# Kernel optimization log

Hardware: AMD Instinct MI355X
Metric: run time of the kernel (lower is better)

Reference implementation:

```python
import jax, jax.numpy as jnp
import numpy as np

D = 128            # EMBEDDING_DIM
B = 8192           # batch
L = 5              # MAX_PLAYLIST_LENGTH
P = 100            # cross projection dim
F = 15 * D         # concat width = 1920
TABLES = {
    'T_name': 1000001, 'T_collab': 4, 'T_track_uri_can': 2262292,
    'T_n_songs': 6, 'T_n_artists': 6, 'T_n_albums': 6,
    'T_artist_name': 287711, 'T_track_uri_pl': 2262293, 'T_track_name': 1483754,
    'T_duration': 101, 'T_album_name': 571626, 'T_artist_pop': 6,
    'T_followers': 11, 'T_track_pop': 11, 'T_genres': 734685,
}


def setup_inputs() -> dict:
    key = jax.random.key(0)
    ks = iter(jax.random.split(key, 64))
    def ridx(shape, hi):
        return jax.random.randint(next(ks), shape, 0, hi, dtype=jnp.int32)
    inp = {
        'name': ridx((B,), 1000001), 'collaborative': ridx((B,), 4),
        'track_uri_can': ridx((B,), 2262292), 'n_songs_pl': ridx((B,), 6),
        'num_artists_pl': ridx((B,), 6), 'num_albums_pl': ridx((B,), 6),
        'artist_name_pl': ridx((B, L), 287711), 'track_uri_pl': ridx((B, L), 2262293),
        'track_name_pl': ridx((B, L), 1483754), 'duration_ms_songs_pl': ridx((B, L), 101),
        'album_name_pl': ridx((B, L), 571626), 'artist_pop_pl': ridx((B, L), 6),
        'artists_followers_pl': ridx((B, L), 11), 'track_pop_pl': ridx((B, L), 11),
        'artist_genres_pl': ridx((B, L), 734685),
    }
    for nm, rows in TABLES.items():
        inp[nm] = jax.random.normal(next(ks), (rows, D), jnp.float32) * 0.05
    def glorot(k, shp):
        lim = np.sqrt(6.0 / (shp[0] + shp[1])).astype(np.float32)
        return jax.random.uniform(k, shp, jnp.float32, -lim, lim)
    inp['cross_V'] = glorot(next(ks), (F, P))
    inp['cross_U'] = glorot(next(ks), (P, F))
    inp['cross_b'] = jnp.zeros((F,), jnp.float32)
    inp['W0'] = glorot(next(ks), (F, 512)); inp['b0'] = jnp.zeros((512,), jnp.float32)
    inp['W1'] = glorot(next(ks), (512, 256)); inp['b1'] = jnp.zeros((256,), jnp.float32)
    inp['W2'] = glorot(next(ks), (256, 128)); inp['b2'] = jnp.zeros((128,), jnp.float32)
    return inp


def _masked_mean(tab, idx):
    # Embedding(mask_zero=True) + GlobalAveragePooling1D: average over idx != 0
    e = tab[idx]                                   # [B, L, D]
    m = (idx != 0).astype(e.dtype)[..., None]      # [B, L, 1]
    return (e * m).sum(1) / jnp.maximum(m.sum(1), 1.0)


def _forward(name, collaborative, track_uri_can, n_songs_pl, num_artists_pl,
             num_albums_pl, artist_name_pl, track_uri_pl, track_name_pl,
             duration_ms_songs_pl, album_name_pl, artist_pop_pl,
             artists_followers_pl, track_pop_pl, artist_genres_pl,
             T_name, T_collab, T_track_uri_can, T_n_songs, T_n_artists,
             T_n_albums, T_artist_name, T_track_uri_pl, T_track_name,
             T_duration, T_album_name, T_artist_pop, T_followers, T_track_pop,
             T_genres, cross_V, cross_U, cross_b, W0, b0, W1, b1, W2, b2):
    all_embs = jnp.concatenate([
        T_name[name], T_collab[collaborative], T_track_uri_can[track_uri_can],
        T_n_songs[n_songs_pl], T_n_artists[num_artists_pl], T_n_albums[num_albums_pl],
        _masked_mean(T_artist_name, artist_name_pl),
        _masked_mean(T_track_uri_pl, track_uri_pl),
        _masked_mean(T_track_name, track_name_pl),
        _masked_mean(T_duration, duration_ms_songs_pl),
        _masked_mean(T_album_name, album_name_pl),
        T_artist_pop[artist_pop_pl].mean(1),        # mask_zero=False -> plain mean
        T_followers[artists_followers_pl].mean(1),
        T_track_pop[track_pop_pl].mean(1),
        _masked_mean(T_genres, artist_genres_pl),
    ], axis=1)                                      # [B, 1920]
    # tfrs DCN Cross (low-rank): x0 * (U(V(x)) + b) + x, x0 == x here
    x0 = all_embs
    cross = x0 * (jnp.dot(jnp.dot(x0, cross_V), cross_U) + cross_b) + x0
    # dense tower (dropout is identity at inference)
    h = jax.nn.relu(cross @ W0 + b0)
    h = jax.nn.relu(h @ W1 + b1)
    h = h @ W2 + b2
    # tf.nn.l2_normalize(x, 1, epsilon=1e-12)
    return h * jax.lax.rsqrt(jnp.maximum(jnp.sum(h * h, 1, keepdims=True), 1e-12))


def reference(name, collaborative, track_uri_can, n_songs_pl, num_artists_pl,
              num_albums_pl, artist_name_pl, track_uri_pl, track_name_pl,
              duration_ms_songs_pl, album_name_pl, artist_pop_pl,
              artists_followers_pl, track_pop_pl, artist_genres_pl,
              T_name, T_collab, T_track_uri_can, T_n_songs, T_n_artists,
              T_n_albums, T_artist_name, T_track_uri_pl, T_track_name,
              T_duration, T_album_name, T_artist_pop, T_followers, T_track_pop,
              T_genres, cross_V, cross_U, cross_b, W0, b0, W1, b1, W2, b2):
    return _forward(name, collaborative, track_uri_can, n_songs_pl, num_artists_pl,
                    num_albums_pl, artist_name_pl, track_uri_pl, track_name_pl,
                    duration_ms_songs_pl, album_name_pl, artist_pop_pl,
                    artists_followers_pl, track_pop_pl, artist_genres_pl,
                    T_name, T_collab, T_track_uri_can, T_n_songs, T_n_artists,
                    T_n_albums, T_artist_name, T_track_uri_pl, T_track_name,
                    T_duration, T_album_name, T_artist_pop, T_followers,
                    T_track_pop, T_genres, cross_V, cross_U, cross_b,
                    W0, b0, W1, b1, W2, b2)
```

## Files before the change

kernel.cpp:

```cpp
#include <hip/hip_runtime.h>


constexpr int B_ = 8192;
constexpr int D_ = 128;
constexpr int L_ = 5;
constexpr int F_ = 1920;
constexpr int P_ = 100;

typedef __attribute__((ext_vector_type(8))) short short8;
typedef __attribute__((ext_vector_type(4))) float f32x4;
typedef __attribute__((ext_vector_type(4))) unsigned short u16x4;

__device__ __forceinline__ unsigned short f2bf(float x) {
  union { float f; unsigned int u; } v; v.f = x;
  unsigned int r = v.u + 0x7FFF + ((v.u >> 16) & 1);
  return (unsigned short)(r >> 16);
}
__device__ __forceinline__ float bf2f(unsigned short b) {
  union { unsigned int u; float f; } v; v.u = ((unsigned int)b) << 16;
  return v.f;
}

__device__ __forceinline__ void gload_lds16(const void* g, void* l) {
  __builtin_amdgcn_global_load_lds(
      (const __attribute__((address_space(1))) void*)g,
      (__attribute__((address_space(3))) void*)l, 16, 0, 0);
}

struct GatherArgs {
  const int*   idx[15];
  const float* tab[15];
};
struct TransBatch {
  const float* src[5];
  unsigned short* dst[5];
  int R[5], C[5], Cpad[5], Rpad[5], tiles_c[5], tile0[6];
};

constexpr int NGATHER = B_ / 8;

__global__ __launch_bounds__(256)
void prep_kernel(GatherArgs ga, unsigned short* __restrict__ X, TransBatch tb) {
  __shared__ float tile[32][33];
  if ((int)blockIdx.x < NGATHER) {
    const int g = threadIdx.x >> 5;
    const int c = threadIdx.x & 31;
    const int b = blockIdx.x * 8 + g;
    unsigned short* xr = X + (size_t)b * F_;
#pragma unroll
    for (int s = 0; s < 6; ++s) {
      const int i = ga.idx[s][b];
      const float4 e = ((const float4*)(ga.tab[s] + (size_t)i * D_))[c];
      u16x4 o; o[0] = f2bf(e.x); o[1] = f2bf(e.y); o[2] = f2bf(e.z); o[3] = f2bf(e.w);
      *(u16x4*)(xr + s * D_ + c * 4) = o;
    }
#pragma unroll
    for (int s = 6; s < 15; ++s) {
      const bool masked = (s < 11) || (s == 14);
      const int* ip = ga.idx[s] + b * L_;
      float sx = 0.f, sy = 0.f, sz = 0.f, sw = 0.f, cnt = 0.f;
#pragma unroll
      for (int l = 0; l < L_; ++l) {
        const int i = ip[l];
        const float4 e = ((const float4*)(ga.tab[s] + (size_t)i * D_))[c];
        if (!masked || i != 0) { sx += e.x; sy += e.y; sz += e.z; sw += e.w; cnt += 1.f; }
      }
      const float inv = 1.f / (masked ? fmaxf(cnt, 1.f) : (float)L_);
      u16x4 o; o[0] = f2bf(sx * inv); o[1] = f2bf(sy * inv);
      o[2] = f2bf(sz * inv); o[3] = f2bf(sw * inv);
      *(u16x4*)(xr + s * D_ + c * 4) = o;
    }
  } else {
    const int id = blockIdx.x - NGATHER;
    int d = 0;
#pragma unroll
    for (int i = 1; i < 5; ++i) if (id >= tb.tile0[i]) d = i;
    const int lid = id - tb.tile0[d];
    const int tcn = tb.tiles_c[d];
    const int tr = lid / tcn, tc = lid - tr * tcn;
    const float* src = tb.src[d];
    unsigned short* dst = tb.dst[d];
    const int R = tb.R[d], C = tb.C[d], Cpad = tb.Cpad[d], Rpad = tb.Rpad[d];
    const int r0 = tr * 32, c0 = tc * 32;
    const int tx = threadIdx.x & 31, ty = threadIdx.x >> 5;
#pragma unroll
    for (int i = 0; i < 32; i += 8) {
      const int r = r0 + ty + i, c = c0 + tx;
      tile[ty + i][tx] = (r < R && c < C) ? src[(size_t)r * C + c] : 0.f;
    }
    __syncthreads();
#pragma unroll
    for (int i = 0; i < 32; i += 8) {
      const int c = c0 + ty + i, r = r0 + tx;
      if (c < Cpad && r < Rpad)
        dst[(size_t)c * Rpad + r] = f2bf(tile[tx][ty + i]);
    }
  }
}

template<int EPI, int BM, int BN, bool DBUF>
__global__ __launch_bounds__(256)
void mfma_gemm(const unsigned short* __restrict__ A, const unsigned short* __restrict__ Bt,
               const float* __restrict__ bias, float* __restrict__ Cf,
               unsigned short* __restrict__ Cb, int M, int N, int K, int Nvalid)
{
  constexpr int BK = 64;
  constexpr int NB = DBUF ? 2 : 1;
  constexpr int WM = BM / 2, WN = BN / 2;
  constexpr int NFM = WM / 16, NFN = WN / 16;
  __shared__ __align__(16) unsigned short As[NB][BM * BK];
  __shared__ __align__(16) unsigned short Bs[NB][BN * BK];

  const int nwg  = gridDim.x * gridDim.y;
  const int wgid = blockIdx.y * gridDim.x + blockIdx.x;
  const int q    = nwg >> 3;
  const int sid  = (wgid & 7) * q + (wgid >> 3);
  const int bx   = sid % gridDim.x, by = sid / gridDim.x;

  const int tid  = threadIdx.x;
  const int wave = tid >> 6, lane = tid & 63;
  const int row0 = by * BM;
  const int n0   = bx * BN;
  const int wr = (wave >> 1) * WM, wc = (wave & 1) * WN;
  const int srow = lane >> 3;
  const int gc   = (lane & 7) ^ srow;

  f32x4 acc[NFM][NFN];
#pragma unroll
  for (int m = 0; m < NFM; ++m)
#pragma unroll
    for (int n = 0; n < NFN; ++n)
      acc[m][n] = (f32x4){0.f, 0.f, 0.f, 0.f};

  const size_t abase = (size_t)(row0 + srow) * K + (size_t)gc * 8;
  const size_t bbase = (size_t)(n0   + srow) * K + (size_t)gc * 8;

  auto stage = [&](int buf, int k0) {
#pragma unroll
    for (int i = 0; i < BM / 32; ++i) {
      const int s = wave * (BM / 32) + i;
      gload_lds16(A + abase + (size_t)s * 8 * K + k0, As[buf] + s * 512);
    }
#pragma unroll
    for (int i = 0; i < BN / 32; ++i) {
      const int s = wave * (BN / 32) + i;
      gload_lds16(Bt + bbase + (size_t)s * 8 * K + k0, Bs[buf] + s * 512);
    }
  };

  auto compute = [&](int buf) {
#pragma unroll
    for (int ks = 0; ks < 2; ++ks) {
      short8 af[NFM], bfr[NFN];
#pragma unroll
      for (int m = 0; m < NFM; ++m) {
        const int r  = wr + m * 16 + (lane & 15);
        const int cs = (ks * 4 + (lane >> 4)) ^ (r & 7);
        af[m] = *(const short8*)(As[buf] + r * 64 + cs * 8);
      }
#pragma unroll
      for (int n = 0; n < NFN; ++n) {
        const int r  = wc + n * 16 + (lane & 15);
        const int cs = (ks * 4 + (lane >> 4)) ^ (r & 7);
        bfr[n] = *(const short8*)(Bs[buf] + r * 64 + cs * 8);
      }
#pragma unroll
      for (int m = 0; m < NFM; ++m)
#pragma unroll
        for (int n = 0; n < NFN; ++n)
          acc[m][n] = __builtin_amdgcn_mfma_f32_16x16x32_bf16(af[m], bfr[n], acc[m][n], 0, 0, 0);
    }
  };

  const int nk = K / BK;
  if (!DBUF) {
    for (int t = 0; t < nk; ++t) {
      stage(0, t * BK);
      __syncthreads();
      compute(0);
      __syncthreads();
    }
  } else {
    stage(0, 0);
    __syncthreads();
    int cur = 0;
    for (int t = 0; t + 1 < nk; ++t) {
      stage(cur ^ 1, (t + 1) * BK);
      compute(cur);
      __syncthreads();
      cur ^= 1;
    }
    compute(cur);
  }

  const int l15 = lane & 15, l4 = lane >> 4;
#pragma unroll
  for (int m = 0; m < NFM; ++m) {
#pragma unroll
    for (int n = 0; n < NFN; ++n) {
      const int col = n0 + wc + n * 16 + l15;
      const float bv = (EPI == 2) ? 0.f : bias[col];
#pragma unroll
      for (int r = 0; r < 4; ++r) {
        const int row = row0 + wr + m * 16 + l4 * 4 + r;
        const float v = acc[m][n][r];
        if (EPI == 0) {
          Cf[(size_t)row * N + col] = v + bv;
        } else if (EPI == 1) {
          Cb[(size_t)row * N + col] = f2bf(fmaxf(v + bv, 0.f));
        } else if (EPI == 2) {
          Cb[(size_t)row * N + col] = (col < Nvalid) ? f2bf(v) : (unsigned short)0;
        } else {
          const float x = bf2f(Cb[(size_t)row * N + col]);
          Cb[(size_t)row * N + col] = f2bf(fmaf(x, v + bv, x));
        }
      }
    }
  }
}

__global__ __launch_bounds__(256)
void l2norm_kernel(const float* __restrict__ H, float* __restrict__ out) {
  const int w    = threadIdx.x >> 6;
  const int lane = threadIdx.x & 63;
  const int b    = blockIdx.x * 4 + w;
  const float* hr = H + (size_t)b * 128;
  const float v0 = hr[lane];
  const float v1 = hr[lane + 64];
  float s = v0 * v0 + v1 * v1;
#pragma unroll
  for (int off = 32; off; off >>= 1) s += __shfl_xor(s, off);
  const float r = rsqrtf(fmaxf(s, 1e-12f));
  out[(size_t)b * 128 + lane]      = v0 * r;
  out[(size_t)b * 128 + lane + 64] = v1 * r;
}

extern "C" void kernel_launch(void* const* d_in, const int* in_sizes, int n_in,
                              void* d_out, int out_size, void* d_ws, size_t ws_size,
                              hipStream_t stream)
{
  GatherArgs ga;
  for (int s = 0; s < 15; ++s) {
    ga.idx[s] = (const int*)d_in[s];
    ga.tab[s] = (const float*)d_in[15 + s];
  }
  const float* cross_V = (const float*)d_in[30];
  const float* cross_U = (const float*)d_in[31];
  const float* cross_b = (const float*)d_in[32];
  const float* W0 = (const float*)d_in[33];
  const float* b0 = (const float*)d_in[34];
  const float* W1 = (const float*)d_in[35];
  const float* b1 = (const float*)d_in[36];
  const float* W2 = (const float*)d_in[37];
  const float* b2 = (const float*)d_in[38];

  char* w = (char*)d_ws;
  unsigned short* Xb  = (unsigned short*)w; w += (size_t)B_ * F_ * 2;
  unsigned short* t   = (unsigned short*)w; w += (size_t)B_ * 128 * 2;
  unsigned short* h0  = (unsigned short*)w; w += (size_t)B_ * 512 * 2;
  unsigned short* h1  = (unsigned short*)w; w += (size_t)B_ * 256 * 2;
  float*          h2  = (float*)w;          w += (size_t)B_ * 128 * 4;
  unsigned short* Vt  = (unsigned short*)w; w += (size_t)128 * F_ * 2;
  unsigned short* Ut  = (unsigned short*)w; w += (size_t)F_ * 128 * 2;
  unsigned short* Wt0 = (unsigned short*)w; w += (size_t)512 * F_ * 2;
  unsigned short* Wt1 = (unsigned short*)w; w += (size_t)256 * 512 * 2;
  unsigned short* Wt2 = (unsigned short*)w; w += (size_t)128 * 256 * 2;

  const dim3 tb(256);

  TransBatch tbt;
  const float* srcs[5] = {cross_V, cross_U, W0, W1, W2};
  unsigned short* dsts[5] = {Vt, Ut, Wt0, Wt1, Wt2};
  const int Rs[5]  = {F_, P_, F_, 512, 256};
  const int Cs[5]  = {P_, F_, 512, 256, 128};
  const int Cp[5]  = {128, F_, 512, 256, 128};
  const int Rp[5]  = {F_, 128, F_, 512, 256};
  int acc_t = 0;
  for (int i = 0; i < 5; ++i) {
    tbt.src[i] = srcs[i]; tbt.dst[i] = dsts[i];
    tbt.R[i] = Rs[i]; tbt.C[i] = Cs[i]; tbt.Cpad[i] = Cp[i]; tbt.Rpad[i] = Rp[i];
    tbt.tiles_c[i] = Cp[i] / 32;
    tbt.tile0[i] = acc_t;
    acc_t += (Rp[i] / 32) * (Cp[i] / 32);
  }
  tbt.tile0[5] = acc_t;

  prep_kernel<<<NGATHER + acc_t, tb, 0, stream>>>(ga, Xb, tbt);
  mfma_gemm<2, 32, 64, true><<<dim3(2, B_ / 32), tb, 0, stream>>>(
      Xb, Vt, nullptr, nullptr, t, B_, 128, F_, P_);
  mfma_gemm<3, 128, 128, false><<<dim3(F_ / 128, B_ / 128), tb, 0, stream>>>(
      t, Ut, cross_b, nullptr, Xb, B_, F_, 128, F_);
  mfma_gemm<1, 64, 64, true><<<dim3(512 / 64, B_ / 64), tb, 0, stream>>>(
      Xb, Wt0, b0, nullptr, h0, B_, 512, F_, 512);
  mfma_gemm<1, 64, 64, true><<<dim3(256 / 64, B_ / 64), tb, 0, stream>>>(
      h0, Wt1, b1, nullptr, h1, B_, 256, 512, 256);
  mfma_gemm<0, 32, 64, true><<<dim3(128 / 64, B_ / 32), tb, 0, stream>>>(
      h1, Wt2, b2, h2, nullptr, B_, 128, 256, 128);
  l2norm_kernel<<<B_ / 4, tb, 0, stream>>>(h2, (float*)d_out);
}
```

Measured before the change: 125.6 us.

## Restructure embedding gather to one block per row with async LDS loads

The gather part of the prep kernel now uses one block per batch row instead of eight rows per block. A first phase computes all 51 row addresses into shared memory. A second phase issues them as direct global-to-LDS 16-byte loads, and a third phase pools, converts to bf16 and writes 16-byte vectors. The aim is more memory-level parallelism for the random embedding reads and wider output stores. The cost is more blocks, two barriers per row, and a larger shared-memory footprint, which could lower occupancy.

Result: no change. 124.7 us (-0.7%).

```diff
diff --git a/kernel.cpp b/kernel.cpp
--- a/kernel.cpp
+++ b/kernel.cpp
@@ -6,10 +6,10 @@
 constexpr int L_ = 5;
 constexpr int F_ = 1920;
 constexpr int P_ = 100;
+constexpr int NLOOK = 51;
 
 typedef __attribute__((ext_vector_type(8))) short short8;
 typedef __attribute__((ext_vector_type(4))) float f32x4;
-typedef __attribute__((ext_vector_type(4))) unsigned short u16x4;
 
 __device__ __forceinline__ unsigned short f2bf(float x) {
   union { float f; unsigned int u; } v; v.f = x;
@@ -37,41 +37,81 @@
   int R[5], C[5], Cpad[5], Rpad[5], tiles_c[5], tile0[6];
 };
 
-constexpr int NGATHER = B_ / 8;
+constexpr int SMEM_RAW   = 52 * 512;
+constexpr int SMEM_ADDR  = SMEM_RAW;
+constexpr int SMEM_IVAL  = SMEM_ADDR + 52 * 8;
+constexpr int SMEM_BYTES = SMEM_IVAL + 52 * 4;
 
 __global__ __launch_bounds__(256)
 void prep_kernel(GatherArgs ga, unsigned short* __restrict__ X, TransBatch tb) {
-  __shared__ float tile[32][33];
-  if ((int)blockIdx.x < NGATHER) {
-    const int g = threadIdx.x >> 5;
-    const int c = threadIdx.x & 31;
-    const int b = blockIdx.x * 8 + g;
-    unsigned short* xr = X + (size_t)b * F_;
-#pragma unroll
-    for (int s = 0; s < 6; ++s) {
-      const int i = ga.idx[s][b];
-      const float4 e = ((const float4*)(ga.tab[s] + (size_t)i * D_))[c];
-      u16x4 o; o[0] = f2bf(e.x); o[1] = f2bf(e.y); o[2] = f2bf(e.z); o[3] = f2bf(e.w);
-      *(u16x4*)(xr + s * D_ + c * 4) = o;
-    }
-#pragma unroll
-    for (int s = 6; s < 15; ++s) {
-      const bool masked = (s < 11) || (s == 14);
-      const int* ip = ga.idx[s] + b * L_;
-      float sx = 0.f, sy = 0.f, sz = 0.f, sw = 0.f, cnt = 0.f;
-#pragma unroll
-      for (int l = 0; l < L_; ++l) {
-        const int i = ip[l];
-        const float4 e = ((const float4*)(ga.tab[s] + (size_t)i * D_))[c];
-        if (!masked || i != 0) { sx += e.x; sy += e.y; sz += e.z; sw += e.w; cnt += 1.f; }
-      }
-      const float inv = 1.f / (masked ? fmaxf(cnt, 1.f) : (float)L_);
-      u16x4 o; o[0] = f2bf(sx * inv); o[1] = f2bf(sy * inv);
-      o[2] = f2bf(sz * inv); o[3] = f2bf(sw * inv);
-      *(u16x4*)(xr + s * D_ + c * 4) = o;
+  __shared__ __align__(16) char smem[SMEM_BYTES];
+  if ((int)blockIdx.x < B_) {
+    const int b = blockIdx.x;
+    const int t = threadIdx.x;
+    float* rawf = (float*)smem;
+    unsigned long long* addrs = (unsigned long long*)(smem + SMEM_ADDR);
+    int* ivals = (int*)(smem + SMEM_IVAL);
+
+    if (t < NLOOK) {
+      int s, l;
+      if (t < 6) { s = t; l = 0; }
+      else { const int p = t - 6; s = 6 + p / 5; l = p - (p / 5) * 5; }
+      const int* ip = nullptr; const float* tp = nullptr;
+#pragma unroll
+      for (int ss = 0; ss < 15; ++ss)
+        if (ss == s) { ip = ga.idx[ss]; tp = ga.tab[ss]; }
+      const int iv = (t < 6) ? ip[b] : ip[b * L_ + l];
+      addrs[t] = (unsigned long long)(tp + (size_t)iv * D_);
+      ivals[t] = iv;
+    }
+    __syncthreads();
+
+    {
+      const int wave = t >> 6, lane = t & 63;
+      for (int j = wave; j < 26; j += 4) {
+        const int lid = 2 * j + (lane >> 5);
+        if (lid < NLOOK) {
+          const char* g = (const char*)addrs[lid] + (size_t)(lane & 31) * 16;
+          gload_lds16(g, smem + j * 1024);
+        }
+      }
+    }
+    __syncthreads();
+
+    if (t < 240) {
+      const int s  = t >> 4;
+      const int d0 = (t & 15) * 8;
+      float v[8];
+      if (s < 6) {
+#pragma unroll
+        for (int jj = 0; jj < 8; ++jj) v[jj] = rawf[s * 128 + d0 + jj];
+      } else {
+        const bool masked = (s < 11) || (s == 14);
+        const int pl0 = 6 + (s - 6) * 5;
+        float cnt = 0.f;
+#pragma unroll
+        for (int jj = 0; jj < 8; ++jj) v[jj] = 0.f;
+#pragma unroll
+        for (int l = 0; l < L_; ++l) {
+          const int iv = ivals[pl0 + l];
+          if (!masked || iv != 0) {
+            cnt += 1.f;
+#pragma unroll
+            for (int jj = 0; jj < 8; ++jj) v[jj] += rawf[(pl0 + l) * 128 + d0 + jj];
+          }
+        }
+        const float inv = 1.f / (masked ? fmaxf(cnt, 1.f) : (float)L_);
+#pragma unroll
+        for (int jj = 0; jj < 8; ++jj) v[jj] *= inv;
+      }
+      short8 o;
+#pragma unroll
+      for (int jj = 0; jj < 8; ++jj) o[jj] = (short)f2bf(v[jj]);
+      *(short8*)(X + (size_t)b * F_ + t * 8) = o;
     }
   } else {
-    const int id = blockIdx.x - NGATHER;
+    float (*tile)[33] = (float(*)[33])smem;
+    const int id = blockIdx.x - B_;
     int d = 0;
 #pragma unroll
     for (int i = 1; i < 5; ++i) if (id >= tb.tile0[i]) d = i;
@@ -285,7 +325,7 @@
   }
   tbt.tile0[5] = acc_t;
 
-  prep_kernel<<<NGATHER + acc_t, tb, 0, stream>>>(ga, Xb, tbt);
+  prep_kernel<<<B_ + acc_t, tb, 0, stream>>>(ga, Xb, tbt);
   mfma_gemm<2, 32, 64, true><<<dim3(2, B_ / 32), tb, 0, stream>>>(
       Xb, Vt, nullptr, nullptr, t, B_, 128, F_, P_);
   mfma_gemm<3, 128, 128, false><<<dim3(F_ / 128, B_ / 128), tb, 0, stream>>>(
```
